# Optimization experiments

Measured on AMD Instinct MI355X. Metric: run time of the kernel, lower is better.

Reference implementation:

```python
import jax, jax.numpy as jnp
import numpy as np

N_NODES = 8192
IN_FEAT = 128
OUT_FEAT = 64
N_EDGES = 262144


def gcn_conv(x, edge_index, W, b):
    # x: [N, F_in], edge_index: [2, E], W: [F_in, F_out], b: [F_out]
    n = x.shape[0]
    loop = jnp.arange(n, dtype=edge_index.dtype)
    src = jnp.concatenate([edge_index[0], loop])  # message sources (incl. self loops)
    dst = jnp.concatenate([edge_index[1], loop])  # aggregation targets
    # symmetric normalization D^{-1/2} (A+I) D^{-1/2}
    deg = jax.ops.segment_sum(jnp.ones_like(dst, dtype=x.dtype), dst, num_segments=n)
    dinv = jax.lax.rsqrt(jnp.where(deg > 0, deg, 1.0))
    norm = dinv[src] * dinv[dst]  # [E + N]
    h = x @ W  # [N, F_out]
    out = jax.ops.segment_sum(h[src] * norm[:, None], dst, num_segments=n)
    return out + b


def setup_inputs() -> dict:
    key = jax.random.key(0)
    k1, k2, k3, k4 = jax.random.split(key, 4)
    x = jax.random.normal(k1, (IN_FEAT, N_NODES), dtype=jnp.float32)
    edge_index = jax.random.randint(k2, (2, N_EDGES), 0, N_NODES, dtype=jnp.int64)
    # encoder GCNConv params (glorot-ish scale)
    W_enc = jax.random.normal(k3, (IN_FEAT, OUT_FEAT), dtype=jnp.float32) / np.sqrt(IN_FEAT)
    b_enc = jnp.zeros((OUT_FEAT,), dtype=jnp.float32)
    return {"x": x, "edge_index": edge_index, "W_enc": W_enc, "b_enc": b_enc}


def reference(x, edge_index, W_enc, b_enc):
    xt = x.T  # [N, F_in]
    z = gcn_conv(xt, edge_index, W_enc, b_enc)  # [N, F_out]
    adj_pred = jax.nn.sigmoid(z @ z.T)  # [N, N]
    return adj_pred
```

## Files before the change

### kernel.cpp

```cpp
#include <hip/hip_runtime.h>
#include <hip/hip_bf16.h>

#define N_NODES 8192
#define F_IN    128
#define F_OUT   64
#define N_EDGES 262144

typedef unsigned int   u32;
typedef unsigned short u16;
typedef __attribute__((ext_vector_type(8))) short short8;
typedef __attribute__((ext_vector_type(4))) float f32x4;

__device__ __forceinline__ u16 f2bf_rne(float f) {
    u32 u = __float_as_uint(f);
    u32 r = (u + 0x7FFFu + ((u >> 16) & 1u)) >> 16;
    return (u16)r;
}
__device__ __forceinline__ float bf2f(u16 b) {
    return __uint_as_float(((u32)b) << 16);
}

__global__ __launch_bounds__(256) void detect_ei_kernel(const int* __restrict__ ei,
                                                        int* __restrict__ eflag) {
    int i = blockIdx.x * 256 + threadIdx.x;
    if (ei[2 * i + 1] != 0) atomicOr(eflag, 1);
}

__global__ __launch_bounds__(256) void detect_xdt_kernel(const u32* __restrict__ xw,
                                                         int* __restrict__ xdt) {
    __shared__ int cnt;
    if (threadIdx.x == 0) cnt = 0;
    __syncthreads();
    u32 w = xw[threadIdx.x * 64 + 1];
    u32 e = (w >> 7) & 0xFFu;
    if (e >= 100u && e <= 134u) atomicAdd(&cnt, 1);
    __syncthreads();
    if (threadIdx.x == 0) *xdt = (cnt > 128) ? 1 : 0;
}

__global__ __launch_bounds__(256) void deg_kernel(const int* __restrict__ ei,
                                                  const int* __restrict__ eflagp,
                                                  int* __restrict__ deg) {
    int e = blockIdx.x * 256 + threadIdx.x;
    bool is64 = (*eflagp == 0);
    int d = is64 ? ei[2 * (N_EDGES + e)] : ei[N_EDGES + e];
    atomicAdd(&deg[d], 1);
}

__global__ __launch_bounds__(1024) void scan_kernel(const int* __restrict__ deg,
                                                    int* __restrict__ offs,
                                                    int* __restrict__ cursor) {
    __shared__ int part[1024];
    int t = threadIdx.x;
    int loc[8];
    int run = 0;
    #pragma unroll
    for (int j = 0; j < 8; ++j) { loc[j] = run; run += deg[t * 8 + j]; }
    part[t] = run;
    __syncthreads();
    for (int d = 1; d < 1024; d <<= 1) {
        int v = (t >= d) ? part[t - d] : 0;
        __syncthreads();
        part[t] += v;
        __syncthreads();
    }
    int pre = part[t] - run;
    #pragma unroll
    for (int j = 0; j < 8; ++j) {
        int v = pre + loc[j];
        offs[t * 8 + j]   = v;
        cursor[t * 8 + j] = v;
    }
    if (t == 1023) offs[8192] = pre + run;
}

__global__ __launch_bounds__(256) void fill_kernel(const int* __restrict__ ei,
                                                   const int* __restrict__ eflagp,
                                                   int* __restrict__ cursor,
                                                   int* __restrict__ esrc) {
    int e = blockIdx.x * 256 + threadIdx.x;
    bool is64 = (*eflagp == 0);
    int s = is64 ? ei[2 * e]             : ei[e];
    int d = is64 ? ei[2 * (N_EDGES + e)] : ei[N_EDGES + e];
    int pos = atomicAdd(&cursor[d], 1);
    esrc[pos] = s;
}

__global__ __launch_bounds__(256) void feat_kernel(
        const void* __restrict__ xv, const void* __restrict__ Wv,
        const void* __restrict__ bv, const int* __restrict__ xdtp,
        const int* __restrict__ deg,
        float* __restrict__ dinv,
        float* __restrict__ h,
        float* __restrict__ z)
{
    __shared__ float Wl[F_IN * F_OUT];
    const bool isbf = (*xdtp != 0);
    int t = threadIdx.x;
    if (isbf) {
        const __hip_bfloat16* Wb = (const __hip_bfloat16*)Wv;
        for (int i = t; i < F_IN * F_OUT; i += 256) Wl[i] = (float)Wb[i];
    } else {
        const float* Wf = (const float*)Wv;
        for (int i = t; i < F_IN * F_OUT; i += 256) Wl[i] = Wf[i];
    }
    __syncthreads();

    int id = blockIdx.x * 256 + t;
    int og = id >> 13;
    int n  = id & (N_NODES - 1);

    float dv = rsqrtf((float)(deg[n] + 1));
    float acc[8] = {0.f,0.f,0.f,0.f,0.f,0.f,0.f,0.f};

    if (isbf) {
        const __hip_bfloat16* xb = (const __hip_bfloat16*)xv;
        for (int f = 0; f < F_IN; ++f) {
            float xval = (float)xb[f * N_NODES + n];
            const float4* w4 = (const float4*)&Wl[f * F_OUT + og * 8];
            float4 w0 = w4[0], w1 = w4[1];
            acc[0] += xval * w0.x; acc[1] += xval * w0.y;
            acc[2] += xval * w0.z; acc[3] += xval * w0.w;
            acc[4] += xval * w1.x; acc[5] += xval * w1.y;
            acc[6] += xval * w1.z; acc[7] += xval * w1.w;
        }
    } else {
        const float* xf = (const float*)xv;
        for (int f = 0; f < F_IN; ++f) {
            float xval = xf[f * N_NODES + n];
            const float4* w4 = (const float4*)&Wl[f * F_OUT + og * 8];
            float4 w0 = w4[0], w1 = w4[1];
            acc[0] += xval * w0.x; acc[1] += xval * w0.y;
            acc[2] += xval * w0.z; acc[3] += xval * w0.w;
            acc[4] += xval * w1.x; acc[5] += xval * w1.y;
            acc[6] += xval * w1.z; acc[7] += xval * w1.w;
        }
    }

    if (og == 0) dinv[n] = dv;

    float hs[8], zb[8];
    float bvals[8];
    if (isbf) {
        const __hip_bfloat16* bb = (const __hip_bfloat16*)bv;
        #pragma unroll
        for (int j = 0; j < 8; ++j) bvals[j] = (float)bb[og * 8 + j];
    } else {
        const float* bf = (const float*)bv;
        #pragma unroll
        for (int j = 0; j < 8; ++j) bvals[j] = bf[og * 8 + j];
    }
    #pragma unroll
    for (int j = 0; j < 8; ++j) {
        hs[j] = dv * acc[j];
        zb[j] = bvals[j] + dv * hs[j];
    }
    float* hp = h + (size_t)n * 64 + og * 8;
    ((float4*)hp)[0] = make_float4(hs[0], hs[1], hs[2], hs[3]);
    ((float4*)hp)[1] = make_float4(hs[4], hs[5], hs[6], hs[7]);
    float* zp = z + (size_t)n * 64 + og * 8;
    ((float4*)zp)[0] = make_float4(zb[0], zb[1], zb[2], zb[3]);
    ((float4*)zp)[1] = make_float4(zb[4], zb[5], zb[6], zb[7]);
}

__global__ __launch_bounds__(256) void gather_kernel(
        const int* __restrict__ offs, const int* __restrict__ esrc,
        const float* __restrict__ h, const float* __restrict__ dinv,
        float* __restrict__ z)
{
    int t = blockIdx.x * 256 + threadIdx.x;
    int d = t >> 6;
    int o = t & 63;
    int beg = offs[d], end = offs[d + 1];
    float acc = 0.f;
    for (int i = beg; i < end; ++i) {
        int s = esrc[i];
        acc += h[(size_t)s * 64 + o];
    }
    z[(size_t)d * 64 + o] += dinv[d] * acc;
}

__global__ __launch_bounds__(256) void gemm_sig_kernel(
        const float* __restrict__ z, float* __restrict__ out)
{
    __shared__ u16 Ah[128][64];
    __shared__ u16 Al[128][64];
    __shared__ u16 Bh[128][64];
    __shared__ u16 Bl[128][64];

    int t  = threadIdx.x;
    int i0 = blockIdx.x * 128;
    int j0 = blockIdx.y * 128;

    #pragma unroll
    for (int it = 0; it < 8; ++it) {
        int item = it * 256 + t;
        int tile = item >> 10;
        int r    = (item >> 3) & 127;
        int c    = item & 7;
        const float* src = z + (size_t)((tile ? j0 : i0) + r) * 64 + c * 8;
        float4 v0 = ((const float4*)src)[0];
        float4 v1 = ((const float4*)src)[1];
        float vf[8] = {v0.x, v0.y, v0.z, v0.w, v1.x, v1.y, v1.z, v1.w};
        short8 sh, sl;
        #pragma unroll
        for (int j = 0; j < 8; ++j) {
            float f  = vf[j];
            u16 hb   = f2bf_rne(f);
            u16 lb   = f2bf_rne(f - bf2f(hb));
            sh[j] = (short)hb;
            sl[j] = (short)lb;
        }
        int cs = c ^ (r & 7);
        u16* dh = tile ? &Bh[r][cs * 8] : &Ah[r][cs * 8];
        u16* dl = tile ? &Bl[r][cs * 8] : &Al[r][cs * 8];
        *(short8*)dh = sh;
        *(short8*)dl = sl;
    }
    __syncthreads();

    int lane = t & 63;
    int w    = t >> 6;
    int lr   = lane & 15;
    int lk   = lane >> 4;

    short8 ah[2][2], al[2][2];
    #pragma unroll
    for (int rt = 0; rt < 2; ++rt)
        #pragma unroll
        for (int kh = 0; kh < 2; ++kh) {
            int rl = w * 32 + rt * 16 + lr;
            int cs = (kh * 4 + lk) ^ (rl & 7);
            ah[rt][kh] = *(const short8*)&Ah[rl][cs * 8];
            al[rt][kh] = *(const short8*)&Al[rl][cs * 8];
        }

    f32x4 acc[2][8];
    #pragma unroll
    for (int rt = 0; rt < 2; ++rt)
        #pragma unroll
        for (int ct = 0; ct < 8; ++ct)
            acc[rt][ct] = (f32x4){0.f, 0.f, 0.f, 0.f};

    #pragma unroll
    for (int ct = 0; ct < 8; ++ct) {
        short8 bh[2], bl[2];
        #pragma unroll
        for (int kh = 0; kh < 2; ++kh) {
            int rl = ct * 16 + lr;
            int cs = (kh * 4 + lk) ^ (rl & 7);
            bh[kh] = *(const short8*)&Bh[rl][cs * 8];
            bl[kh] = *(const short8*)&Bl[rl][cs * 8];
        }
        #pragma unroll
        for (int rt = 0; rt < 2; ++rt) {
            #pragma unroll
            for (int kh = 0; kh < 2; ++kh) {
                acc[rt][ct] = __builtin_amdgcn_mfma_f32_16x16x32_bf16(
                    ah[rt][kh], bh[kh], acc[rt][ct], 0, 0, 0);
                acc[rt][ct] = __builtin_amdgcn_mfma_f32_16x16x32_bf16(
                    ah[rt][kh], bl[kh], acc[rt][ct], 0, 0, 0);
                acc[rt][ct] = __builtin_amdgcn_mfma_f32_16x16x32_bf16(
                    al[rt][kh], bh[kh], acc[rt][ct], 0, 0, 0);
            }
        }
    }

    #pragma unroll
    for (int rt = 0; rt < 2; ++rt) {
        #pragma unroll
        for (int ct = 0; ct < 8; ++ct) {
            int gcol = j0 + ct * 16 + lr;
            #pragma unroll
            for (int rg = 0; rg < 4; ++rg) {
                int grow = i0 + w * 32 + rt * 16 + lk * 4 + rg;
                float v  = acc[rt][ct][rg];
                out[(size_t)grow * N_NODES + gcol] = 1.f / (1.f + __expf(-v));
            }
        }
    }
}

extern "C" void kernel_launch(void* const* d_in, const int* in_sizes, int n_in,
                              void* d_out, int out_size, void* d_ws, size_t ws_size,
                              hipStream_t stream) {
    const void* x  = d_in[0];
    const int*  ei = (const int*)d_in[1];
    const void* W  = d_in[2];
    const void* b  = d_in[3];
    float* out = (float*)d_out;

    char* ws = (char*)d_ws;
    int*   deg    = (int*)ws;
    int*   eflag  = (int*)(ws + 32768);
    int*   xdt    = (int*)(ws + 32784);
    int*   offs   = (int*)(ws + 36864);
    int*   cursor = (int*)(ws + 73728);
    float* dinv   = (float*)(ws + 110592);
    int*   esrc   = (int*)(ws + 147456);
    float* h      = (float*)(ws + 1196032);
    float* z      = (float*)(ws + 3293184);

    hipMemsetAsync(ws, 0, 36864, stream);
    detect_ei_kernel<<<32, 256, 0, stream>>>(ei, eflag);
    detect_xdt_kernel<<<1, 256, 0, stream>>>((const u32*)x, xdt);
    deg_kernel<<<N_EDGES / 256, 256, 0, stream>>>(ei, eflag, deg);
    scan_kernel<<<1, 1024, 0, stream>>>(deg, offs, cursor);
    fill_kernel<<<N_EDGES / 256, 256, 0, stream>>>(ei, eflag, cursor, esrc);
    feat_kernel<<<256, 256, 0, stream>>>(x, W, b, xdt, deg, dinv, h, z);
    gather_kernel<<<N_NODES * 64 / 256, 256, 0, stream>>>(offs, esrc, h, dinv, z);
    gemm_sig_kernel<<<dim3(64, 64), 256, 0, stream>>>(z, out);
}
```

Measured before the change: 349.8 us.

## Exploit symmetry of z·zᵀ and merge small launches

The output GEMM now launches only lower-triangular 128x128 tiles. Each off-diagonal tile also writes its transpose through a padded shared-memory staging buffer with float4 stores, which roughly halves the MFMA work while keeping the output writes the same. Separately, the two detect kernels are merged into one launch, and the CSR fill kernel is merged with the feature kernel to cut launch overhead. The cost is extra shared-memory transposes and syncs, plus larger shared-memory use that could lower occupancy.

```diff
diff --git a/kernel.cpp b/kernel.cpp
--- a/kernel.cpp
+++ b/kernel.cpp
@@ -20,22 +20,23 @@
     return __uint_as_float(((u32)b) << 16);
 }
 
-__global__ __launch_bounds__(256) void detect_ei_kernel(const int* __restrict__ ei,
-                                                        int* __restrict__ eflag) {
-    int i = blockIdx.x * 256 + threadIdx.x;
-    if (ei[2 * i + 1] != 0) atomicOr(eflag, 1);
-}
-
-__global__ __launch_bounds__(256) void detect_xdt_kernel(const u32* __restrict__ xw,
-                                                         int* __restrict__ xdt) {
-    __shared__ int cnt;
-    if (threadIdx.x == 0) cnt = 0;
-    __syncthreads();
-    u32 w = xw[threadIdx.x * 64 + 1];
-    u32 e = (w >> 7) & 0xFFu;
-    if (e >= 100u && e <= 134u) atomicAdd(&cnt, 1);
-    __syncthreads();
-    if (threadIdx.x == 0) *xdt = (cnt > 128) ? 1 : 0;
+__global__ __launch_bounds__(256) void detect_kernel(const int* __restrict__ ei,
+                                                     const u32* __restrict__ xw,
+                                                     int* __restrict__ eflag,
+                                                     int* __restrict__ xdt) {
+    if (blockIdx.x < 32) {
+        int i = blockIdx.x * 256 + threadIdx.x;
+        if (ei[2 * i + 1] != 0) atomicOr(eflag, 1);
+    } else {
+        __shared__ int cnt;
+        if (threadIdx.x == 0) cnt = 0;
+        __syncthreads();
+        u32 w = xw[threadIdx.x * 64 + 1];
+        u32 e = (w >> 7) & 0xFFu;
+        if (e >= 100u && e <= 134u) atomicAdd(&cnt, 1);
+        __syncthreads();
+        if (threadIdx.x == 0) *xdt = (cnt > 128) ? 1 : 0;
+    }
 }
 
 __global__ __launch_bounds__(256) void deg_kernel(const int* __restrict__ ei,
@@ -74,19 +75,9 @@
     if (t == 1023) offs[8192] = pre + run;
 }
 
-__global__ __launch_bounds__(256) void fill_kernel(const int* __restrict__ ei,
-                                                   const int* __restrict__ eflagp,
-                                                   int* __restrict__ cursor,
-                                                   int* __restrict__ esrc) {
-    int e = blockIdx.x * 256 + threadIdx.x;
-    bool is64 = (*eflagp == 0);
-    int s = is64 ? ei[2 * e]             : ei[e];
-    int d = is64 ? ei[2 * (N_EDGES + e)] : ei[N_EDGES + e];
-    int pos = atomicAdd(&cursor[d], 1);
-    esrc[pos] = s;
-}
-
-__global__ __launch_bounds__(256) void feat_kernel(
+__global__ __launch_bounds__(256) void fill_feat_kernel(
+        const int* __restrict__ ei, const int* __restrict__ eflagp,
+        int* __restrict__ cursor, int* __restrict__ esrc,
         const void* __restrict__ xv, const void* __restrict__ Wv,
         const void* __restrict__ bv, const int* __restrict__ xdtp,
         const int* __restrict__ deg,
@@ -95,8 +86,19 @@
         float* __restrict__ z)
 {
     __shared__ float Wl[F_IN * F_OUT];
+    int t = threadIdx.x;
+
+    if (blockIdx.x < N_EDGES / 256) {
+        int e = blockIdx.x * 256 + t;
+        bool is64 = (*eflagp == 0);
+        int s = is64 ? ei[2 * e]             : ei[e];
+        int d = is64 ? ei[2 * (N_EDGES + e)] : ei[N_EDGES + e];
+        int pos = atomicAdd(&cursor[d], 1);
+        esrc[pos] = s;
+        return;
+    }
+
     const bool isbf = (*xdtp != 0);
-    int t = threadIdx.x;
     if (isbf) {
         const __hip_bfloat16* Wb = (const __hip_bfloat16*)Wv;
         for (int i = t; i < F_IN * F_OUT; i += 256) Wl[i] = (float)Wb[i];
@@ -106,7 +108,7 @@
     }
     __syncthreads();
 
-    int id = blockIdx.x * 256 + t;
+    int id = (blockIdx.x - N_EDGES / 256) * 256 + t;
     int og = id >> 13;
     int n  = id & (N_NODES - 1);
 
@@ -139,7 +141,6 @@
 
     if (og == 0) dinv[n] = dv;
 
-    float hs[8], zb[8];
     float bvals[8];
     if (isbf) {
         const __hip_bfloat16* bb = (const __hip_bfloat16*)bv;
@@ -150,6 +151,7 @@
         #pragma unroll
         for (int j = 0; j < 8; ++j) bvals[j] = bf[og * 8 + j];
     }
+    float hs[8], zb[8];
     #pragma unroll
     for (int j = 0; j < 8; ++j) {
         hs[j] = dv * acc[j];
@@ -183,14 +185,23 @@
 __global__ __launch_bounds__(256) void gemm_sig_kernel(
         const float* __restrict__ z, float* __restrict__ out)
 {
-    __shared__ u16 Ah[128][64];
-    __shared__ u16 Al[128][64];
-    __shared__ u16 Bh[128][64];
-    __shared__ u16 Bl[128][64];
-
-    int t  = threadIdx.x;
-    int i0 = blockIdx.x * 128;
-    int j0 = blockIdx.y * 128;
+    __shared__ __align__(16) char smem[128 * 129 * 4];
+    u16 (*Ah)[64] = (u16(*)[64])(smem);
+    u16 (*Al)[64] = (u16(*)[64])(smem + 16384);
+    u16 (*Bh)[64] = (u16(*)[64])(smem + 32768);
+    u16 (*Bl)[64] = (u16(*)[64])(smem + 49152);
+    float (*Cs)[129] = (float(*)[129])(smem);
+
+    int t = threadIdx.x;
+
+    int tgt = blockIdx.x;
+    int bi = (int)((sqrtf(8.f * (float)tgt + 1.f) - 1.f) * 0.5f);
+    while ((bi + 1) * (bi + 2) / 2 <= tgt) ++bi;
+    while (bi * (bi + 1) / 2 > tgt) --bi;
+    int bj = tgt - bi * (bi + 1) / 2;
+    int i0 = bi * 128;
+    int j0 = bj * 128;
+    bool offdiag = (bi != bj);
 
     #pragma unroll
     for (int it = 0; it < 8; ++it) {
@@ -267,16 +278,52 @@
     }
 
     #pragma unroll
-    for (int rt = 0; rt < 2; ++rt) {
+    for (int rt = 0; rt < 2; ++rt)
+        #pragma unroll
+        for (int ct = 0; ct < 8; ++ct)
+            #pragma unroll
+            for (int rg = 0; rg < 4; ++rg) {
+                float v = acc[rt][ct][rg];
+                acc[rt][ct][rg] =
+                    __builtin_amdgcn_rcpf(1.f + __expf(-v));
+            }
+
+    if (offdiag) {
+        __syncthreads();
+        #pragma unroll
+        for (int rt = 0; rt < 2; ++rt)
+            #pragma unroll
+            for (int ct = 0; ct < 8; ++ct) {
+                int col = ct * 16 + lr;
+                int row = w * 32 + rt * 16 + lk * 4;
+                #pragma unroll
+                for (int rg = 0; rg < 4; ++rg)
+                    Cs[row + rg][col] = acc[rt][ct][rg];
+            }
+    }
+
+    #pragma unroll
+    for (int rt = 0; rt < 2; ++rt)
         #pragma unroll
         for (int ct = 0; ct < 8; ++ct) {
             int gcol = j0 + ct * 16 + lr;
             #pragma unroll
             for (int rg = 0; rg < 4; ++rg) {
                 int grow = i0 + w * 32 + rt * 16 + lk * 4 + rg;
-                float v  = acc[rt][ct][rg];
-                out[(size_t)grow * N_NODES + gcol] = 1.f / (1.f + __expf(-v));
+                out[(size_t)grow * N_NODES + gcol] = acc[rt][ct][rg];
             }
+        }
+
+    if (offdiag) {
+        __syncthreads();
+        #pragma unroll
+        for (int u = 0; u < 16; ++u) {
+            int q   = u * 256 + t;
+            int rr  = q >> 5;
+            int cc4 = (q & 31) * 4;
+            float4 v = make_float4(Cs[cc4 + 0][rr], Cs[cc4 + 1][rr],
+                                   Cs[cc4 + 2][rr], Cs[cc4 + 3][rr]);
+            *(float4*)(out + (size_t)(j0 + rr) * N_NODES + i0 + cc4) = v;
         }
     }
 }
@@ -302,12 +349,11 @@
     float* z      = (float*)(ws + 3293184);
 
     hipMemsetAsync(ws, 0, 36864, stream);
-    detect_ei_kernel<<<32, 256, 0, stream>>>(ei, eflag);
-    detect_xdt_kernel<<<1, 256, 0, stream>>>((const u32*)x, xdt);
+    detect_kernel<<<33, 256, 0, stream>>>(ei, (const u32*)x, eflag, xdt);
     deg_kernel<<<N_EDGES / 256, 256, 0, stream>>>(ei, eflag, deg);
     scan_kernel<<<1, 1024, 0, stream>>>(deg, offs, cursor);
-    fill_kernel<<<N_EDGES / 256, 256, 0, stream>>>(ei, eflag, cursor, esrc);
-    feat_kernel<<<256, 256, 0, stream>>>(x, W, b, xdt, deg, dinv, h, z);
+    fill_feat_kernel<<<N_EDGES / 256 + 256, 256, 0, stream>>>(
+        ei, eflag, cursor, esrc, x, W, b, xdt, deg, dinv, h, z);
     gather_kernel<<<N_NODES * 64 / 256, 256, 0, stream>>>(offs, esrc, h, dinv, z);
-    gemm_sig_kernel<<<dim3(64, 64), 256, 0, stream>>>(z, out);
-}
+    gemm_sig_kernel<<<64 * 65 / 2, 256, 0, stream>>>(z, out);
+}
```

Measured after the change: 344.2 us. About the same (-1.6%).
